# Kernel tuning notes

Hardware: AMD Instinct MI355X
Metric: run time of the kernel (lower is better)

Reference implementation:

```python
import jax, jax.numpy as jnp
import numpy as np
from functools import partial

N = 512
H, W = 324, 332
C = 120
NEAR, FAR, BG = 0.01, 100.0, 1.0


def setup_inputs() -> dict:
    key = jax.random.key(0)
    k1, k2, k3, k4, k5, k6 = jax.random.split(key, 6)
    # positions: small xy, depth z in [2, 8] so everything projects on screen
    xy = 0.5 * jax.random.normal(k1, (N, 2), dtype=jnp.float32)
    z = jax.random.uniform(k2, (N, 1), dtype=jnp.float32, minval=2.0, maxval=8.0)
    positions = jnp.concatenate([xy, z], axis=-1)  # [N,3]
    rotations = jax.random.normal(k3, (N, 4), dtype=jnp.float32)  # unused by the math
    # scales in [0.5, 4.5] pixels -> small footprints, early-break never triggers
    scales = jax.random.uniform(k4, (N, 3), dtype=jnp.float32) * 4.0 + 0.5
    opacities = jax.random.uniform(k5, (N,), dtype=jnp.float32)
    spectral_features = jax.random.uniform(k6, (N, C), dtype=jnp.float32)
    tone_mapping = jnp.ones((C,), dtype=jnp.float32)
    intrinsics = jnp.array([[300.0, 0.0, 166.0],
                            [0.0, 300.0, 162.0],
                            [0.0, 0.0, 1.0]], dtype=jnp.float32)
    extrinsics = jnp.eye(4, dtype=jnp.float32)
    return {"positions": positions, "rotations": rotations, "scales": scales,
            "opacities": opacities, "spectral_features": spectral_features,
            "tone_mapping": tone_mapping, "intrinsics": intrinsics,
            "extrinsics": extrinsics}


def _render(positions, scales, opacities, spectral_features, tone_mapping,
            intrinsics, extrinsics):
    # --- projection (world -> camera -> screen) ---
    ph = jnp.concatenate([positions, jnp.ones_like(positions[:, :1])], axis=-1)  # [N,4]
    cam = ph @ extrinsics.T                     # [N,4]
    cam3 = cam[:, :3]
    proj = cam3 @ intrinsics.T                  # [N,3]
    screen = proj[:, :2] / (proj[:, 2:3] + 1e-6)  # [N,2] (x, y)
    depths = cam3[:, 2]                         # [N]

    # --- frustum / screen culling mask (kept as a validity flag) ---
    valid = (depths > NEAR) & (depths < FAR)
    valid &= (screen[:, 0] > -100.0) & (screen[:, 0] < W + 100.0)
    valid &= (screen[:, 1] > -100.0) & (screen[:, 1] < H + 100.0)

    # --- 2D covariance: diag(scale_x^2, scale_y^2), regularized inverse ---
    s2 = scales[:, :2] ** 2
    cov = jnp.zeros((positions.shape[0], 2, 2), dtype=positions.dtype)
    cov = cov.at[:, 0, 0].set(s2[:, 0]).at[:, 1, 1].set(s2[:, 1])
    cov_inv = jnp.linalg.inv(cov + 1e-4 * jnp.eye(2, dtype=positions.dtype))  # [N,2,2]

    # --- depth sort (front to back) ---
    order = jnp.argsort(depths)
    screen_s = screen[order]
    depths_s = depths[order]
    cinv_s = cov_inv[order]
    op_s = opacities[order]
    valid_s = valid[order]
    spec_s = spectral_features[order]           # [N,C]

    # pixel grid: pix[h,w] = (x=w, y=h)
    X, Y = jnp.meshgrid(jnp.arange(W), jnp.arange(H))  # each [H,W]
    pix = jnp.stack([X, Y], axis=-1).astype(positions.dtype)  # [H,W,2]

    def step(A, g):
        pos, cinv, op, v = g
        done = jnp.mean(A) > 0.99  # torch early-break condition
        off = (pos[0] < -W) | (pos[0] > 2 * W) | (pos[1] < -H) | (pos[1] > 2 * H)
        skip = done | off | jnp.logical_not(v)
        diff = pix - pos                                    # [H,W,2]
        mahal = jnp.einsum('hwi,ij,hwj->hw', diff, cinv, diff)
        alpha = op * jnp.exp(-0.5 * mahal) * (1.0 - A)      # [H,W]
        alpha = jnp.where(skip, 0.0, alpha)
        return A + alpha, alpha

    A0 = jnp.zeros((H, W), dtype=positions.dtype)
    A_final, alphas = jax.lax.scan(step, A0, (screen_s, cinv_s, op_s, valid_s))  # alphas [N,H,W]

    # spectral/depth accumulation == sum_i feature_i * alpha_i (GEMM over N)
    spectral = jnp.einsum('nc,nhw->chw', spec_s, alphas)    # [C,H,W]
    depth_img = jnp.einsum('n,nhw->hw', depths_s, alphas)   # [H,W]
    spectral = spectral + BG * (1.0 - A_final)[None]
    spectral = spectral * tone_mapping[:, None, None]
    return spectral, depth_img, A_final


def reference(positions, rotations, scales, opacities, spectral_features,
              tone_mapping, intrinsics, extrinsics):
    # rotations are accepted but unused by the original math (diagonal 2D cov)
    return _render(positions, scales, opacities, spectral_features,
                   tone_mapping, intrinsics, extrinsics)
```

## Files before the change

### kernel.cpp

```cpp
#include <hip/hip_runtime.h>
#include <math.h>

#define N_G 512
#define IMG_H 324
#define IMG_W 332
#define N_C 120
#define HW (IMG_H*IMG_W)
#define CHUNK 24
#define TSX 21
#define TSY 81
#define NT (TSX*TSY)


__global__ __launch_bounds__(256, 4) void k_render(
    const float* __restrict__ pos, const float* __restrict__ scales,
    const float* __restrict__ opac, const float* __restrict__ Km,
    const float* __restrict__ Em, const float* __restrict__ spec,
    const float* __restrict__ tm, float* __restrict__ out)
{
  __shared__ float prm[N_G*8];
  __shared__ float buf[CHUNK*64];
  __shared__ float sbuf[CHUNK*N_C];
  __shared__ float Tcar[64], Dcar[64];
  __shared__ unsigned int livem[4];
  __shared__ int wcnt[4];
  __shared__ int stopf;

  const int tid  = threadIdx.x;
  const int w    = tid >> 6;
  const int lane = tid & 63;
  const int tx = lane & 15, ty = lane >> 4;
  const unsigned long long ltm = (1ull << lane) - 1ull;

  float psx[2], psy[2], pc00[2], pc11[2], pl2[2], pd[2];
  float bxmin[2], bxmax[2], bymin[2], bymax[2];
  {
    const float E0=Em[0],E1=Em[1],E2=Em[2],E3=Em[3],
                E4=Em[4],E5=Em[5],E6=Em[6],E7=Em[7],
                E8=Em[8],E9=Em[9],E10=Em[10],E11=Em[11];
    const float K0=Km[0],K1=Km[1],K2=Km[2],
                K3=Km[3],K4=Km[4],K5=Km[5],
                K6=Km[6],K7=Km[7],K8=Km[8];
    #pragma unroll
    for (int q = 0; q < 2; ++q) {
      const int g = w*128 + lane + q*64;
      float p0 = pos[g*3+0], p1 = pos[g*3+1], p2 = pos[g*3+2];
      float cam0 = E0*p0 + E1*p1 + E2*p2  + E3;
      float cam1 = E4*p0 + E5*p1 + E6*p2  + E7;
      float cam2 = E8*p0 + E9*p1 + E10*p2 + E11;
      float pr0 = K0*cam0 + K1*cam1 + K2*cam2;
      float pr1 = K3*cam0 + K4*cam1 + K5*cam2;
      float pr2 = K6*cam0 + K7*cam1 + K8*cam2;
      float inv = 1.0f/(pr2 + 1e-6f);
      float sx = pr0*inv, sy = pr1*inv;
      float depth = cam2;
      bool valid = (depth > 0.01f) && (depth < 100.0f)
                && (sx > -100.0f) && (sx < (float)IMG_W + 100.0f)
                && (sy > -100.0f) && (sy < (float)IMG_H + 100.0f);
      bool off = (sx < -(float)IMG_W) || (sx > 2.0f*(float)IMG_W)
              || (sy < -(float)IMG_H) || (sy > 2.0f*(float)IMG_H);
      bool skip = off || (!valid);
      float s0 = scales[g*3+0], s1 = scales[g*3+1];
      float v0 = s0*s0 + 1e-4f, v1 = s1*s1 + 1e-4f;
      const float HL2E = 0.72134752f;
      psx[q] = sx; psy[q] = sy;
      pc00[q] = HL2E/v0; pc11[q] = HL2E/v1;
      pl2[q] = __log2f(skip ? 0.0f : opac[g]);
      pd[q]  = depth;
      float rx = 6.0f*sqrtf(v0);
      float ry = 6.0f*sqrtf(v1);
      bxmin[q] = skip ?  1e9f : sx - rx;
      bxmax[q] = skip ? -1e9f : sx + rx;
      bymin[q] = skip ?  1e9f : sy - ry;
      bymax[q] = skip ? -1e9f : sy + ry;
    }
  }

  const int t = blockIdx.x;
  const int jx = t % TSX, ky = t / TSX;
  const int bx = 10 + ((jx & 1) ? ((jx+1)>>1) : -((jx+1)>>1));
  const int by = 40 + ((ky & 1) ? ((ky+1)>>1) : -((ky+1)>>1));

  const int x = bx*16 + tx;
  const int y = by*4 + ty;
  const bool inb = (x < IMG_W) && (y < IMG_H);
  const float px = (float)min(x, IMG_W-1);
  const float py = (float)min(y, IMG_H-1);
  const float wxmin = (float)(bx*16), wxmax = wxmin + 15.0f;
  const float wymin = (float)(by*4),  wymax = wymin + 3.0f;

  bool h0 = !(bxmin[0] > wxmax || bxmax[0] < wxmin ||
              bymin[0] > wymax || bymax[0] < wymin);
  bool h1 = !(bxmin[1] > wxmax || bxmax[1] < wxmin ||
              bymin[1] > wymax || bymax[1] < wymin);
  unsigned long long m0 = __ballot(h0), m1 = __ballot(h1);
  int c0 = __popcll(m0);
  if (lane == 0) wcnt[w] = c0 + __popcll(m1);
  if (tid == 0) stopf = 0;
  __syncthreads();
  int offw = 0;
  #pragma unroll
  for (int k = 0; k < 4; ++k) if (k < w) offw += wcnt[k];
  const int nh = wcnt[0] + wcnt[1] + wcnt[2] + wcnt[3];
  const int p0 = offw + __popcll(m0 & ltm);
  const int p1 = offw + c0 + __popcll(m1 & ltm);
  if (h0) buf[p0] = pd[0];
  if (h1) buf[p1] = pd[1];
  if (tid < 4) buf[nh + tid] = 1e30f;
  __syncthreads();

  if (h0 | h1) {
    int r0 = 0, r1 = 0;
    const float d0 = pd[0], d1 = pd[1];
    for (int j = 0; j < nh; j += 4) {
      float4 k4 = *(const float4*)&buf[j];
      if (h0) {
        r0 += (k4.x < d0 || (k4.x == d0 && j+0 < p0)) ? 1 : 0;
        r0 += (k4.y < d0 || (k4.y == d0 && j+1 < p0)) ? 1 : 0;
        r0 += (k4.z < d0 || (k4.z == d0 && j+2 < p0)) ? 1 : 0;
        r0 += (k4.w < d0 || (k4.w == d0 && j+3 < p0)) ? 1 : 0;
      }
      if (h1) {
        r1 += (k4.x < d1 || (k4.x == d1 && j+0 < p1)) ? 1 : 0;
        r1 += (k4.y < d1 || (k4.y == d1 && j+1 < p1)) ? 1 : 0;
        r1 += (k4.z < d1 || (k4.z == d1 && j+2 < p1)) ? 1 : 0;
        r1 += (k4.w < d1 || (k4.w == d1 && j+3 < p1)) ? 1 : 0;
      }
    }
    if (h0) {
      *(float4*)&prm[r0*8]   = make_float4(psx[0], psy[0], pc00[0], pc11[0]);
      *(float4*)&prm[r0*8+4] = make_float4(pl2[0], pd[0],
                                 __int_as_float((w*128 + lane)*N_C), 0.0f);
    }
    if (h1) {
      *(float4*)&prm[r1*8]   = make_float4(psx[1], psy[1], pc00[1], pc11[1]);
      *(float4*)&prm[r1*8+4] = make_float4(pl2[1], pd[1],
                                 __int_as_float((w*128 + lane + 64)*N_C), 0.0f);
    }
  }
  __syncthreads();

  float T = 1.0f, dacc = 0.0f;
  float4 acc[8] = {};

  for (int cb = 0; cb < nh; cb += CHUNK) {
    if (stopf) break;
    const int nc = min(CHUNK, nh - cb);

    unsigned int lm = 0;
    #pragma unroll 2
    for (int j = w; j < nc; j += 4) {
      float4 q0 = *(const float4*)&prm[(cb+j)*8];
      float4 q1 = *(const float4*)&prm[(cb+j)*8+4];
      float dx = px - q0.x, dy = py - q0.y;
      float m = q0.z*dx*dx + q0.w*dy*dy;
      float e = q1.x - m;
      buf[j*64 + lane] = exp2f(e);
      unsigned long long bl = __ballot(e > -24.0f);
      if (bl) {
        lm |= 1u << j;
        int sbase = __float_as_int(q1.z);
        sbuf[j*N_C + lane] = spec[sbase + lane];
        if (lane < N_C - 64) sbuf[j*N_C + 64 + lane] = spec[sbase + 64 + lane];
      }
    }
    if (lane == 0) livem[w] = lm;
    __syncthreads();
    const unsigned int mask = livem[0] | livem[1] | livem[2] | livem[3];

    if (w == 0) {
      unsigned int mb = mask;
      while (mb) {
        const int j = __builtin_ctz(mb); mb &= mb - 1;
        float a  = buf[j*64 + lane];
        float wv = a * T;
        buf[j*64 + lane] = wv;
        dacc = fmaf(prm[(cb+j)*8+5], wv, dacc);
        T *= (1.0f - a);
      }
      unsigned long long alive = __ballot(T >= 1e-5f);
      if (lane == 0 && alive == 0ull) stopf = 1;
    }
    __syncthreads();

    unsigned int m2 = mask;
    while (m2) {
      const int j = __builtin_ctz(m2); m2 &= m2 - 1;
      float wv = buf[j*64 + lane];
      const float* base = &sbuf[j*N_C];
      #pragma unroll
      for (int gi = 0; gi < 8; ++gi) {
        const int g = w + 4*gi;
        if (g < 30) {
          float4 s4 = *(const float4*)(base + 4*g);
          acc[gi].x = fmaf(wv, s4.x, acc[gi].x);
          acc[gi].y = fmaf(wv, s4.y, acc[gi].y);
          acc[gi].z = fmaf(wv, s4.z, acc[gi].z);
          acc[gi].w = fmaf(wv, s4.w, acc[gi].w);
        }
      }
    }
    __syncthreads();
  }

  if (w == 0) { Tcar[lane] = T; Dcar[lane] = dacc; }
  __syncthreads();

  if (inb) {
    const int pixi = y*IMG_W + x;
    const float bgT = Tcar[lane];
    #pragma unroll
    for (int gi = 0; gi < 8; ++gi) {
      const int g = w + 4*gi;
      if (g < 30) {
        float4 t4 = *(const float4*)&tm[4*g];
        out[(4*g+0)*HW + pixi] = (acc[gi].x + bgT)*t4.x;
        out[(4*g+1)*HW + pixi] = (acc[gi].y + bgT)*t4.y;
        out[(4*g+2)*HW + pixi] = (acc[gi].z + bgT)*t4.z;
        out[(4*g+3)*HW + pixi] = (acc[gi].w + bgT)*t4.w;
      }
    }
    if (w == 0) out[N_C*HW + pixi] = Dcar[lane];
    if (w == 1) out[N_C*HW + HW + pixi] = 1.0f - Tcar[lane];
  }
}

extern "C" void kernel_launch(void* const* d_in, const int* in_sizes, int n_in,
                              void* d_out, int out_size, void* d_ws, size_t ws_size,
                              hipStream_t stream) {
  const float* pos    = (const float*)d_in[0];
  const float* scales = (const float*)d_in[2];
  const float* opac   = (const float*)d_in[3];
  const float* spec   = (const float*)d_in[4];
  const float* tm     = (const float*)d_in[5];
  const float* K      = (const float*)d_in[6];
  const float* E      = (const float*)d_in[7];
  float* out = (float*)d_out;
  (void)d_ws; (void)ws_size;

  k_render<<<NT, 256, 0, stream>>>(pos, scales, opac, K, E, spec, tm, out);
}
```

Before: 131.7 us.

## Split spectral channels across four blocks per tile to raise parallelism

Each pixel tile is now handled by four blocks, and each block accumulates a quarter of the 120 spectral channels (interleaved float4 groups). The per-chunk spectral staging into shared memory shrinks to 32 floats per gaussian, and the chunk size doubles to 48 with 64-bit live masks. Projection, binning, depth sorting and the transmittance scan are repeated in every one of the four blocks, adding redundant work in exchange for four times as many blocks and fewer accumulator registers.

```diff
diff --git a/kernel.cpp b/kernel.cpp
--- a/kernel.cpp
+++ b/kernel.cpp
@@ -6,10 +6,11 @@
 #define IMG_W 332
 #define N_C 120
 #define HW (IMG_H*IMG_W)
-#define CHUNK 24
+#define CHUNK 48
 #define TSX 21
 #define TSY 81
 #define NT (TSX*TSY)
+#define NBLK (NT*4)
 
 
 __global__ __launch_bounds__(256, 4) void k_render(
@@ -20,9 +21,9 @@
 {
   __shared__ float prm[N_G*8];
   __shared__ float buf[CHUNK*64];
-  __shared__ float sbuf[CHUNK*N_C];
-  __shared__ float Tcar[64], Dcar[64];
-  __shared__ unsigned int livem[4];
+  __shared__ float sbuf[CHUNK*32];
+  __shared__ float Tcar[64];
+  __shared__ unsigned long long livem[4];
   __shared__ int wcnt[4];
   __shared__ int stopf;
 
@@ -31,6 +32,9 @@
   const int lane = tid & 63;
   const int tx = lane & 15, ty = lane >> 4;
   const unsigned long long ltm = (1ull << lane) - 1ull;
+
+  const int t  = blockIdx.x >> 2;
+  const int cq = blockIdx.x & 3;
 
   float psx[2], psy[2], pc00[2], pc11[2], pl2[2], pd[2];
   float bxmin[2], bxmax[2], bymin[2], bymax[2];
@@ -76,7 +80,6 @@
     }
   }
 
-  const int t = blockIdx.x;
   const int jx = t % TSX, ky = t / TSX;
   const int bx = 10 + ((jx & 1) ? ((jx+1)>>1) : -((jx+1)>>1));
   const int by = 40 + ((ky & 1) ? ((ky+1)>>1) : -((ky+1)>>1));
@@ -141,13 +144,17 @@
   __syncthreads();
 
   float T = 1.0f, dacc = 0.0f;
-  float4 acc[8] = {};
+  float4 acc0 = {0,0,0,0}, acc1 = {0,0,0,0};
+  const int g0 = cq + 8*w;
+  const bool g1ok = (g0 + 4) < 30;
+  const int stc = 16*(lane >> 2) + 4*cq + (lane & 3);
+  const bool stok = (lane < 32) && (stc < N_C);
 
   for (int cb = 0; cb < nh; cb += CHUNK) {
     if (stopf) break;
     const int nc = min(CHUNK, nh - cb);
 
-    unsigned int lm = 0;
+    unsigned long long lm = 0;
     #pragma unroll 2
     for (int j = w; j < nc; j += 4) {
       float4 q0 = *(const float4*)&prm[(cb+j)*8];
@@ -158,24 +165,23 @@
       buf[j*64 + lane] = exp2f(e);
       unsigned long long bl = __ballot(e > -24.0f);
       if (bl) {
-        lm |= 1u << j;
+        lm |= 1ull << j;
         int sbase = __float_as_int(q1.z);
-        sbuf[j*N_C + lane] = spec[sbase + lane];
-        if (lane < N_C - 64) sbuf[j*N_C + 64 + lane] = spec[sbase + 64 + lane];
+        if (stok) sbuf[j*32 + lane] = spec[sbase + stc];
       }
     }
     if (lane == 0) livem[w] = lm;
     __syncthreads();
-    const unsigned int mask = livem[0] | livem[1] | livem[2] | livem[3];
+    const unsigned long long mask = livem[0]|livem[1]|livem[2]|livem[3];
 
     if (w == 0) {
-      unsigned int mb = mask;
+      unsigned long long mb = mask;
       while (mb) {
-        const int j = __builtin_ctz(mb); mb &= mb - 1;
+        const int j = __builtin_ctzll(mb); mb &= mb - 1;
         float a  = buf[j*64 + lane];
         float wv = a * T;
         buf[j*64 + lane] = wv;
-        dacc = fmaf(prm[(cb+j)*8+5], wv, dacc);
+        if (cq == 2) dacc = fmaf(prm[(cb+j)*8+5], wv, dacc);
         T *= (1.0f - a);
       }
       unsigned long long alive = __ballot(T >= 1e-5f);
@@ -183,45 +189,48 @@
     }
     __syncthreads();
 
-    unsigned int m2 = mask;
+    unsigned long long m2 = mask;
     while (m2) {
-      const int j = __builtin_ctz(m2); m2 &= m2 - 1;
+      const int j = __builtin_ctzll(m2); m2 &= m2 - 1;
       float wv = buf[j*64 + lane];
-      const float* base = &sbuf[j*N_C];
-      #pragma unroll
-      for (int gi = 0; gi < 8; ++gi) {
-        const int g = w + 4*gi;
-        if (g < 30) {
-          float4 s4 = *(const float4*)(base + 4*g);
-          acc[gi].x = fmaf(wv, s4.x, acc[gi].x);
-          acc[gi].y = fmaf(wv, s4.y, acc[gi].y);
-          acc[gi].z = fmaf(wv, s4.z, acc[gi].z);
-          acc[gi].w = fmaf(wv, s4.w, acc[gi].w);
-        }
+      const float* row = &sbuf[j*32 + 8*w];
+      float4 s0 = *(const float4*)(row);
+      acc0.x = fmaf(wv, s0.x, acc0.x);
+      acc0.y = fmaf(wv, s0.y, acc0.y);
+      acc0.z = fmaf(wv, s0.z, acc0.z);
+      acc0.w = fmaf(wv, s0.w, acc0.w);
+      if (g1ok) {
+        float4 s1 = *(const float4*)(row + 4);
+        acc1.x = fmaf(wv, s1.x, acc1.x);
+        acc1.y = fmaf(wv, s1.y, acc1.y);
+        acc1.z = fmaf(wv, s1.z, acc1.z);
+        acc1.w = fmaf(wv, s1.w, acc1.w);
       }
     }
     __syncthreads();
   }
 
-  if (w == 0) { Tcar[lane] = T; Dcar[lane] = dacc; }
+  if (w == 0) Tcar[lane] = T;
   __syncthreads();
 
   if (inb) {
     const int pixi = y*IMG_W + x;
     const float bgT = Tcar[lane];
-    #pragma unroll
-    for (int gi = 0; gi < 8; ++gi) {
-      const int g = w + 4*gi;
-      if (g < 30) {
-        float4 t4 = *(const float4*)&tm[4*g];
-        out[(4*g+0)*HW + pixi] = (acc[gi].x + bgT)*t4.x;
-        out[(4*g+1)*HW + pixi] = (acc[gi].y + bgT)*t4.y;
-        out[(4*g+2)*HW + pixi] = (acc[gi].z + bgT)*t4.z;
-        out[(4*g+3)*HW + pixi] = (acc[gi].w + bgT)*t4.w;
-      }
-    }
-    if (w == 0) out[N_C*HW + pixi] = Dcar[lane];
-    if (w == 1) out[N_C*HW + HW + pixi] = 1.0f - Tcar[lane];
+    float4 t0 = *(const float4*)&tm[4*g0];
+    out[(4*g0+0)*HW + pixi] = (acc0.x + bgT)*t0.x;
+    out[(4*g0+1)*HW + pixi] = (acc0.y + bgT)*t0.y;
+    out[(4*g0+2)*HW + pixi] = (acc0.z + bgT)*t0.z;
+    out[(4*g0+3)*HW + pixi] = (acc0.w + bgT)*t0.w;
+    if (g1ok) {
+      const int g1 = g0 + 4;
+      float4 t1 = *(const float4*)&tm[4*g1];
+      out[(4*g1+0)*HW + pixi] = (acc1.x + bgT)*t1.x;
+      out[(4*g1+1)*HW + pixi] = (acc1.y + bgT)*t1.y;
+      out[(4*g1+2)*HW + pixi] = (acc1.z + bgT)*t1.z;
+      out[(4*g1+3)*HW + pixi] = (acc1.w + bgT)*t1.w;
+    }
+    if (cq == 2 && w == 0) out[N_C*HW + pixi] = dacc;
+    if (cq == 3 && w == 0) out[N_C*HW + HW + pixi] = 1.0f - bgT;
   }
 }
 
@@ -238,5 +247,5 @@
   float* out = (float*)d_out;
   (void)d_ws; (void)ws_size;
 
-  k_render<<<NT, 256, 0, stream>>>(pos, scales, opac, K, E, spec, tm, out);
+  k_render<<<NBLK, 256, 0, stream>>>(pos, scales, opac, K, E, spec, tm, out);
 }
```

Result: faster. 113.7 us (-13.7%).
